# Optimization experiments

Measured on AMD Instinct MI355X. Metric: run time of the kernel, lower is better.

## Reference

```python
import jax, jax.numpy as jnp
import numpy as np

N_NODES = 100000
N_EDGES = 1600000
F_IN = 128
F_OUT = 64


def setup_inputs() -> dict:
    key = jax.random.key(0)
    kx, kw, kv, ks, kd = jax.random.split(key, 5)
    x = jax.random.normal(kx, (N_NODES, F_IN), dtype=jnp.float32)
    # xavier_uniform init for weight [in, out]
    limit = float(np.sqrt(6.0 / (F_IN + F_OUT)))
    weight = jax.random.uniform(kw, (F_IN, F_OUT), dtype=jnp.float32,
                                minval=-limit, maxval=limit)
    edge_val = jax.random.uniform(kv, (N_EDGES,), dtype=jnp.float32)
    edge_src = jax.random.randint(ks, (N_EDGES,), 0, N_NODES, dtype=jnp.int64)
    edge_dst = jax.random.randint(kd, (N_EDGES,), 0, N_NODES, dtype=jnp.int64)
    return {"x": x, "weight": weight, "edge_val": edge_val,
            "edge_src": edge_src, "edge_dst": edge_dst}


def reference(x, weight, edge_val, edge_src, edge_dst):
    # dropout p = 0.0 -> identity
    support = x @ weight                                  # [N, F_OUT] dense GEMM
    # spmm: out[dst] += val * support[src]  (adj row = dst, col = src)
    messages = support[edge_src] * edge_val[:, None]       # [E, F_OUT] gather
    out = jax.ops.segment_sum(messages, edge_dst,
                              num_segments=x.shape[0])     # [N, F_OUT] scatter-add
    return jax.nn.relu(out)
```

## Files before the change

### kernel.cpp

```cpp
#include <hip/hip_runtime.h>

#define F_IN 128
#define F_OUT 64
#define GROWS 128
#define XBSTRIDE 136

#define NPB 128
#define NPB_SHIFT 7
#define BCAP 800
#define ECAP 2240
#define TILE 8192
#define BSTH 1024
#define TMAX 256

__device__ inline unsigned f2bf(float f) {
    const unsigned u = __float_as_uint(f);
    return (u + 0x7FFFu + ((u >> 16) & 1u)) >> 16;
}
__device__ inline float bf_lo(unsigned u) { return __uint_as_float(u << 16); }
__device__ inline float bf_hi(unsigned u) { return __uint_as_float(u & 0xFFFF0000u); }

using bf16x8 = __attribute__((ext_vector_type(8))) short;
using f32x4  = __attribute__((ext_vector_type(4))) float;

struct GemmSh {
    unsigned short xt[GROWS * XBSTRIDE];
    unsigned short wth[F_OUT * XBSTRIDE];
    unsigned short wtl[F_OUT * XBSTRIDE];
};
struct ScatSh {
    int2 ebuf2[TILE];
    int  h[BCAP];
    int  lcur[BCAP];
    int  wsum[16];
    int  woff[16];
};
union FusedSh { GemmSh g; ScatSh s; };

__global__ __launch_bounds__(BSTH) void fused_kernel(const float* __restrict__ x,
                                                     const float* __restrict__ w,
                                                     unsigned short* __restrict__ support,
                                                     int n_nodes,
                                                     const float* __restrict__ edge_val,
                                                     const int* __restrict__ edge_src,
                                                     const int* __restrict__ edge_dst,
                                                     int* __restrict__ toff,
                                                     int2* __restrict__ sorted,
                                                     int n_edges, int nb, int T) {
    __shared__ FusedSh u;
    const int tid = threadIdx.x;

    if ((int)blockIdx.x >= T) {
        const int row0 = (blockIdx.x - T) * GROWS;

        {
            #pragma unroll
            for (int i = tid; i < F_OUT * (F_IN / 8); i += BSTH) {
                const int col = i & 63;
                const int kb  = (i >> 6) << 3;
                unsigned short sh[8], sl[8];
                #pragma unroll
                for (int j = 0; j < 8; ++j) {
                    const float f = w[(size_t)(kb + j) * F_OUT + col];
                    const unsigned h = f2bf(f);
                    sh[j] = (unsigned short)h;
                    sl[j] = (unsigned short)f2bf(f - __uint_as_float(h << 16));
                }
                uint4 oh, ol;
                oh.x = sh[0] | ((unsigned)sh[1] << 16); oh.y = sh[2] | ((unsigned)sh[3] << 16);
                oh.z = sh[4] | ((unsigned)sh[5] << 16); oh.w = sh[6] | ((unsigned)sh[7] << 16);
                ol.x = sl[0] | ((unsigned)sl[1] << 16); ol.y = sl[2] | ((unsigned)sl[3] << 16);
                ol.z = sl[4] | ((unsigned)sl[5] << 16); ol.w = sl[6] | ((unsigned)sl[7] << 16);
                *(uint4*)&u.g.wth[col * XBSTRIDE + kb] = oh;
                *(uint4*)&u.g.wtl[col * XBSTRIDE + kb] = ol;
            }
        }
        {
            const float4* x4 = (const float4*)x;
            #pragma unroll
            for (int i = tid; i < GROWS * (F_IN / 8); i += BSTH) {
                const int r  = i >> 4;
                const int k8 = i & 15;
                const int row = row0 + r;
                float4 a = make_float4(0.f, 0.f, 0.f, 0.f);
                float4 b = make_float4(0.f, 0.f, 0.f, 0.f);
                if (row < n_nodes) {
                    a = x4[(size_t)row * (F_IN / 4) + 2 * k8 + 0];
                    b = x4[(size_t)row * (F_IN / 4) + 2 * k8 + 1];
                }
                uint4 o;
                o.x = f2bf(a.x) | (f2bf(a.y) << 16);
                o.y = f2bf(a.z) | (f2bf(a.w) << 16);
                o.z = f2bf(b.x) | (f2bf(b.y) << 16);
                o.w = f2bf(b.z) | (f2bf(b.w) << 16);
                *(uint4*)&u.g.xt[r * XBSTRIDE + k8 * 8] = o;
            }
        }
        __syncthreads();

        const int ln = tid & 63;
        const int wv = tid >> 6;
        const int rt = wv >> 1;
        const int cp = (wv & 1) << 1;
        const int lr = ln >> 4;
        const int lc = ln & 15;

        const unsigned short* ar  = &u.g.xt [(rt * 16 + lc) * XBSTRIDE + lr * 8];
        const unsigned short* bh0 = &u.g.wth[(cp * 16 + lc) * XBSTRIDE + lr * 8];
        const unsigned short* bh1 = &u.g.wth[((cp + 1) * 16 + lc) * XBSTRIDE + lr * 8];
        const unsigned short* bl0 = &u.g.wtl[(cp * 16 + lc) * XBSTRIDE + lr * 8];
        const unsigned short* bl1 = &u.g.wtl[((cp + 1) * 16 + lc) * XBSTRIDE + lr * 8];

        f32x4 acc0 = {0.f, 0.f, 0.f, 0.f};
        f32x4 acc1 = {0.f, 0.f, 0.f, 0.f};
        #pragma unroll
        for (int kc = 0; kc < 4; ++kc) {
            const bf16x8 a  = *(const bf16x8*)(ar  + kc * 32);
            const bf16x8 h0 = *(const bf16x8*)(bh0 + kc * 32);
            const bf16x8 h1 = *(const bf16x8*)(bh1 + kc * 32);
            const bf16x8 l0 = *(const bf16x8*)(bl0 + kc * 32);
            const bf16x8 l1 = *(const bf16x8*)(bl1 + kc * 32);
            acc0 = __builtin_amdgcn_mfma_f32_16x16x32_bf16(a, h0, acc0, 0, 0, 0);
            acc1 = __builtin_amdgcn_mfma_f32_16x16x32_bf16(a, h1, acc1, 0, 0, 0);
            acc0 = __builtin_amdgcn_mfma_f32_16x16x32_bf16(a, l0, acc0, 0, 0, 0);
            acc1 = __builtin_amdgcn_mfma_f32_16x16x32_bf16(a, l1, acc1, 0, 0, 0);
        }

        #pragma unroll
        for (int i = 0; i < 4; ++i) {
            const int row = row0 + rt * 16 + lr * 4 + i;
            if (row < n_nodes) {
                unsigned short* sp = &support[(size_t)row * F_OUT + lc];
                sp[cp * 16]       = (unsigned short)f2bf(acc0[i]);
                sp[(cp + 1) * 16] = (unsigned short)f2bf(acc1[i]);
            }
        }
        return;
    }

    const int te  = blockIdx.x * TILE;
    const int cnt = min(TILE, n_edges - te);

    for (int i = tid; i < BCAP; i += BSTH) u.s.h[i] = 0;
    __syncthreads();

    const int cnt4 = cnt >> 2;
    const int4*   s4 = (const int4*)(edge_src + te);
    const int4*   d4 = (const int4*)(edge_dst + te);
    const float4* v4 = (const float4*)(edge_val + te);
    int4 rs[2], rd[2]; float4 rv[2];
    #pragma unroll
    for (int it = 0; it < 2; ++it) {
        const int t = tid + it * BSTH;
        if (t < cnt4) {
            rs[it] = s4[t]; rd[it] = d4[t]; rv[it] = v4[t];
            atomicAdd(&u.s.h[rd[it].x >> NPB_SHIFT], 1);
            atomicAdd(&u.s.h[rd[it].y >> NPB_SHIFT], 1);
            atomicAdd(&u.s.h[rd[it].z >> NPB_SHIFT], 1);
            atomicAdd(&u.s.h[rd[it].w >> NPB_SHIFT], 1);
        }
    }
    if (tid == 0) {
        for (int e = cnt4 << 2; e < cnt; ++e)
            atomicAdd(&u.s.h[edge_dst[te + e] >> NPB_SHIFT], 1);
    }
    __syncthreads();

    const int v = (tid < nb) ? u.s.h[tid] : 0;
    int s = v;
    #pragma unroll
    for (int off = 1; off < 64; off <<= 1) {
        const int t = __shfl_up(s, off, 64);
        if ((tid & 63) >= off) s += t;
    }
    const int wave = tid >> 6;
    if ((tid & 63) == 63) u.s.wsum[wave] = s;
    __syncthreads();
    if (tid < 16) {
        const int ws = u.s.wsum[tid];
        int sc = ws;
        #pragma unroll
        for (int off = 1; off < 16; off <<= 1) {
            const int t = __shfl_up(sc, off, 64);
            if (tid >= off) sc += t;
        }
        u.s.woff[tid] = sc - ws;
    }
    __syncthreads();

    {
        const int bid = blockIdx.x;
        if (tid < nb) {
            const int start = s + u.s.woff[wave] - v;
            u.s.lcur[tid] = start;
            toff[(size_t)tid * T + bid] = start;
        }
        if (tid == 0) toff[(size_t)nb * T + bid] = cnt;
    }
    __syncthreads();

    #pragma unroll
    for (int it = 0; it < 2; ++it) {
        const int t = tid + it * BSTH;
        if (t < cnt4) {
            int b, r;
            b = rd[it].x >> NPB_SHIFT; r = atomicAdd(&u.s.lcur[b], 1);
            u.s.ebuf2[r] = make_int2(rs[it].x | ((rd[it].x & (NPB - 1)) << 20), __float_as_int(rv[it].x));
            b = rd[it].y >> NPB_SHIFT; r = atomicAdd(&u.s.lcur[b], 1);
            u.s.ebuf2[r] = make_int2(rs[it].y | ((rd[it].y & (NPB - 1)) << 20), __float_as_int(rv[it].y));
            b = rd[it].z >> NPB_SHIFT; r = atomicAdd(&u.s.lcur[b], 1);
            u.s.ebuf2[r] = make_int2(rs[it].z | ((rd[it].z & (NPB - 1)) << 20), __float_as_int(rv[it].z));
            b = rd[it].w >> NPB_SHIFT; r = atomicAdd(&u.s.lcur[b], 1);
            u.s.ebuf2[r] = make_int2(rs[it].w | ((rd[it].w & (NPB - 1)) << 20), __float_as_int(rv[it].w));
        }
    }
    if (tid == 0) {
        for (int e = cnt4 << 2; e < cnt; ++e) {
            const int dd = edge_dst[te + e];
            const int b = dd >> NPB_SHIFT;
            const int r = atomicAdd(&u.s.lcur[b], 1);
            u.s.ebuf2[r] = make_int2(edge_src[te + e] | ((dd & (NPB - 1)) << 20),
                                     __float_as_int(edge_val[te + e]));
        }
    }
    __syncthreads();

    for (int k = tid; k < cnt; k += BSTH)
        sorted[(size_t)te + k] = u.s.ebuf2[k];
}

__global__ __launch_bounds__(512) void baccum_kernel(const unsigned short* __restrict__ support,
                                                     const int2* __restrict__ sorted,
                                                     const int* __restrict__ toff,
                                                     float* __restrict__ out,
                                                     int n_nodes, int T, int nb) {
    __shared__ int2 ebuf[ECAP];
    __shared__ int2 ebuf2[ECAP];
    __shared__ int tstart[TMAX];
    __shared__ int toffb[TMAX];
    __shared__ int tlen_s[TMAX];
    __shared__ int wsum3[4];
    __shared__ int total_s;
    __shared__ int hist[NPB];
    __shared__ int node_off[NPB + 1];
    __shared__ int cursor[NPB];
    __shared__ int wsum2[2];

    const int tid = threadIdx.x;
    const int b = blockIdx.x;

    int mycnt = 0, myoff = 0;
    if (tid < TMAX) {
        if (tid < T) {
            const int s0 = toff[(size_t)b * T + tid];
            const int e0 = toff[(size_t)(b + 1) * T + tid];
            toffb[tid] = s0;
            mycnt = e0 - s0;
            tlen_s[tid] = mycnt;
        }
        int s = mycnt;
        #pragma unroll
        for (int off = 1; off < 64; off <<= 1) {
            const int t = __shfl_up(s, off, 64);
            if ((tid & 63) >= off) s += t;
        }
        if ((tid & 63) == 63) wsum3[tid >> 6] = s;
        myoff = s - mycnt;
    }
    __syncthreads();
    if (tid < TMAX && tid < T) {
        int add = 0;
        const int wv = tid >> 6;
        for (int q2 = 0; q2 < wv; ++q2) add += wsum3[q2];
        tstart[tid] = myoff + add;
    }
    if (tid == 0) total_s = wsum3[0] + wsum3[1] + wsum3[2] + wsum3[3];
    __syncthreads();
    const int total = total_s;

    const int g8 = tid >> 3;
    const int q  = tid & 7;
    const uint4* sup = (const uint4*)support;

    float4 accA[2], accB[2];
    #pragma unroll
    for (int j = 0; j < 2; ++j) {
        accA[j] = make_float4(0.f, 0.f, 0.f, 0.f);
        accB[j] = make_float4(0.f, 0.f, 0.f, 0.f);
    }

    auto scan_bins = [&]() {
        int v = 0;
        if (tid < NPB) v = hist[tid];
        int s = v;
        if (tid < NPB) {
            #pragma unroll
            for (int off = 1; off < 64; off <<= 1) {
                const int t = __shfl_up(s, off, 64);
                if ((tid & 63) >= off) s += t;
            }
            if ((tid & 63) == 63) wsum2[tid >> 6] = s;
        }
        __syncthreads();
        if (tid < NPB) {
            const int incl = s + ((tid >= 64) ? wsum2[0] : 0);
            node_off[tid + 1] = incl;
            cursor[tid] = incl - v;
            if (tid == 0) node_off[0] = 0;
        }
    };
    auto gather = [&]() {
        #pragma unroll
        for (int j = 0; j < 2; ++j) {
            const int nl = g8 + 64 * j;
            int k = node_off[nl];
            const int ke = node_off[nl + 1];
            float4 aA = accA[j], aB = accB[j];
            while (k + 8 <= ke) {
                int2 e[8];
                uint4 s8[8];
                #pragma unroll
                for (int u2 = 0; u2 < 8; ++u2) e[u2] = ebuf2[k + u2];
                #pragma unroll
                for (int u2 = 0; u2 < 8; ++u2)
                    s8[u2] = sup[(size_t)(e[u2].x & 0xFFFFF) * 8 + q];
                #pragma unroll
                for (int u2 = 0; u2 < 8; ++u2) {
                    const float v = __int_as_float(e[u2].y);
                    aA.x += v * bf_lo(s8[u2].x); aA.y += v * bf_hi(s8[u2].x);
                    aA.z += v * bf_lo(s8[u2].y); aA.w += v * bf_hi(s8[u2].y);
                    aB.x += v * bf_lo(s8[u2].z); aB.y += v * bf_hi(s8[u2].z);
                    aB.z += v * bf_lo(s8[u2].w); aB.w += v * bf_hi(s8[u2].w);
                }
                k += 8;
            }
            for (; k < ke; ++k) {
                const int2 e0 = ebuf2[k];
                const uint4 s0 = sup[(size_t)(e0.x & 0xFFFFF) * 8 + q];
                const float v0 = __int_as_float(e0.y);
                aA.x += v0 * bf_lo(s0.x); aA.y += v0 * bf_hi(s0.x);
                aA.z += v0 * bf_lo(s0.y); aA.w += v0 * bf_hi(s0.y);
                aB.x += v0 * bf_lo(s0.z); aB.y += v0 * bf_hi(s0.z);
                aB.z += v0 * bf_lo(s0.w); aB.w += v0 * bf_hi(s0.w);
            }
            accA[j] = aA; accB[j] = aB;
        }
    };

    if (total <= ECAP) {
        if (tid < NPB) hist[tid] = 0;
        __syncthreads();

        const int wv = tid >> 6;
        const int ln = tid & 63;

        for (int t = wv; t < T; t += 8) {
            const int len = tlen_s[t];
            const size_t gbase = (size_t)t * TILE + toffb[t];
            for (int j = ln; j < len; j += 64) {
                const int2 ev = sorted[gbase + j];
                atomicAdd(&hist[((unsigned)ev.x) >> 20], 1);
            }
        }
        __syncthreads();

        scan_bins();
        __syncthreads();

        for (int t = wv; t < T; t += 8) {
            const int len = tlen_s[t];
            const size_t gbase = (size_t)t * TILE + toffb[t];
            for (int j = ln; j < len; j += 64) {
                const int2 ev = sorted[gbase + j];
                const int r = atomicAdd(&cursor[((unsigned)ev.x) >> 20], 1);
                ebuf2[r] = ev;
            }
        }
        __syncthreads();

        gather();
    } else {
        for (int cb = 0; cb < total; cb += ECAP) {
            const int cnt = min(ECAP, total - cb);

            __syncthreads();
            if (tid < NPB) hist[tid] = 0;
            __syncthreads();

            for (int i = tid; i < cnt; i += 512) {
                const int g = cb + i;
                int lo = 0, hi = T - 1;
                while (lo < hi) {
                    const int mid = (lo + hi + 1) >> 1;
                    if (tstart[mid] <= g) lo = mid; else hi = mid - 1;
                }
                const int2 ev = sorted[(size_t)lo * TILE + toffb[lo] + (g - tstart[lo])];
                ebuf[i] = ev;
                atomicAdd(&hist[((unsigned)ev.x) >> 20], 1);
            }
            __syncthreads();

            scan_bins();
            __syncthreads();

            for (int i = tid; i < cnt; i += 512) {
                const int2 ev = ebuf[i];
                const int r = atomicAdd(&cursor[((unsigned)ev.x) >> 20], 1);
                ebuf2[r] = ev;
            }
            __syncthreads();

            gather();
        }
    }

    const int base = b << NPB_SHIFT;
    #pragma unroll
    for (int j = 0; j < 2; ++j) {
        const int node = base + g8 + 64 * j;
        if (node < n_nodes) {
            float4 vA = accA[j], vB = accB[j];
            vA.x = fmaxf(vA.x, 0.f); vA.y = fmaxf(vA.y, 0.f);
            vA.z = fmaxf(vA.z, 0.f); vA.w = fmaxf(vA.w, 0.f);
            vB.x = fmaxf(vB.x, 0.f); vB.y = fmaxf(vB.y, 0.f);
            vB.z = fmaxf(vB.z, 0.f); vB.w = fmaxf(vB.w, 0.f);
            ((float4*)out)[(size_t)node * 16 + 2 * q + 0] = vA;
            ((float4*)out)[(size_t)node * 16 + 2 * q + 1] = vB;
        }
    }
}

__global__ __launch_bounds__(256) void scatter_kernel(const unsigned short* __restrict__ support,
                                                      const float* __restrict__ edge_val,
                                                      const int* __restrict__ edge_src,
                                                      const int* __restrict__ edge_dst,
                                                      float* __restrict__ out,
                                                      int n_edges) {
    const long gid = (long)blockIdx.x * blockDim.x + threadIdx.x;
    const int e = (int)(gid >> 4);
    if (e >= n_edges) return;
    const int q = (int)(gid & 15);
    const int src   = edge_src[e];
    const int dst   = edge_dst[e];
    const float val = edge_val[e];
    const uint2 s = ((const uint2*)support)[(size_t)src * 16 + q];
    float* o = &out[(size_t)dst * F_OUT + q * 4];
    atomicAdd(o + 0, val * bf_lo(s.x));
    atomicAdd(o + 1, val * bf_hi(s.x));
    atomicAdd(o + 2, val * bf_lo(s.y));
    atomicAdd(o + 3, val * bf_hi(s.y));
}

__global__ __launch_bounds__(256) void relu_kernel(float* __restrict__ out, int n4) {
    const int i = blockIdx.x * blockDim.x + threadIdx.x;
    if (i < n4) {
        float4 v = ((float4*)out)[i];
        v.x = fmaxf(v.x, 0.f); v.y = fmaxf(v.y, 0.f);
        v.z = fmaxf(v.z, 0.f); v.w = fmaxf(v.w, 0.f);
        ((float4*)out)[i] = v;
    }
}

extern "C" void kernel_launch(void* const* d_in, const int* in_sizes, int n_in,
                              void* d_out, int out_size, void* d_ws, size_t ws_size,
                              hipStream_t stream) {
    const float* x        = (const float*)d_in[0];
    const float* w        = (const float*)d_in[1];
    const float* edge_val = (const float*)d_in[2];
    const int*   edge_src = (const int*)d_in[3];
    const int*   edge_dst = (const int*)d_in[4];
    float* out = (float*)d_out;

    const int n_nodes = in_sizes[0] / F_IN;
    const int n_edges = in_sizes[2];
    const int nb = (n_nodes + NPB - 1) >> NPB_SHIFT;
    const int T  = (n_edges + TILE - 1) / TILE;
    const int G  = (n_nodes + GROWS - 1) / GROWS;

    char* p = (char*)d_ws;
    unsigned short* support = (unsigned short*)p;
    p += (size_t)n_nodes * F_OUT * sizeof(unsigned short);
    p = (char*)(((size_t)p + 15) & ~(size_t)15);
    int2* sorted = (int2*)p;  p += (size_t)T * TILE * sizeof(int2);
    int*  toff   = (int*)p;   p += (size_t)(nb + 1) * T * sizeof(int);
    const size_t ws_needed = (size_t)(p - (char*)d_ws);

    const bool ok = (ws_size >= ws_needed) && (nb <= BCAP) && (n_nodes < (1 << 20))
                    && (T <= TMAX);
    if (ok) {
        fused_kernel<<<T + G, BSTH, 0, stream>>>(x, w, support, n_nodes,
                                                 edge_val, edge_src, edge_dst,
                                                 toff, sorted, n_edges, nb, T);
        baccum_kernel<<<nb, 512, 0, stream>>>(support, sorted, toff, out,
                                              n_nodes, T, nb);
    } else {
        fused_kernel<<<G, BSTH, 0, stream>>>(x, w, support, n_nodes,
                                             edge_val, edge_src, edge_dst,
                                             nullptr, nullptr, n_edges, nb, 0);
        hipMemsetAsync(d_out, 0, (size_t)out_size * sizeof(float), stream);
        const long st = (long)n_edges * 16;
        scatter_kernel<<<(int)((st + 255) / 256), 256, 0, stream>>>(
            support, edge_val, edge_src, edge_dst, out, n_edges);
        const int n4o = out_size / 4;
        relu_kernel<<<(n4o + 255) / 256, 256, 0, stream>>>(out, n4o);
    }
}
```

Baseline: 176.9 us.

## Balance per-node gather with dynamic work queue and flat tile-map edge load

In the common fast path, each block now builds a byte map from edge position to source tile. This lets all threads load edges with a single flat, coalesced loop that reads global memory once into shared memory, instead of reading it twice with per-wave tile loops. The fixed assignment of two nodes per 8-thread group is replaced by an atomic counter, so groups pull nodes dynamically to even out imbalance caused by varying node degree. The tile map is filled serially per tile by one thread each, and the per-node atomic adds a little overhead.

```diff
diff --git a/kernel.cpp b/kernel.cpp
--- a/kernel.cpp
+++ b/kernel.cpp
@@ -236,6 +236,7 @@
                                                      int n_nodes, int T, int nb) {
     __shared__ int2 ebuf[ECAP];
     __shared__ int2 ebuf2[ECAP];
+    __shared__ unsigned char tileof[ECAP];
     __shared__ int tstart[TMAX];
     __shared__ int toffb[TMAX];
     __shared__ int tlen_s[TMAX];
@@ -245,6 +246,7 @@
     __shared__ int node_off[NPB + 1];
     __shared__ int cursor[NPB];
     __shared__ int wsum2[2];
+    __shared__ int next_node;
 
     const int tid = threadIdx.x;
     const int b = blockIdx.x;
@@ -274,20 +276,14 @@
         for (int q2 = 0; q2 < wv; ++q2) add += wsum3[q2];
         tstart[tid] = myoff + add;
     }
-    if (tid == 0) total_s = wsum3[0] + wsum3[1] + wsum3[2] + wsum3[3];
+    if (tid == 0) { total_s = wsum3[0] + wsum3[1] + wsum3[2] + wsum3[3]; next_node = 0; }
     __syncthreads();
     const int total = total_s;
 
     const int g8 = tid >> 3;
     const int q  = tid & 7;
+    const int ln = tid & 63;
     const uint4* sup = (const uint4*)support;
-
-    float4 accA[2], accB[2];
-    #pragma unroll
-    for (int j = 0; j < 2; ++j) {
-        accA[j] = make_float4(0.f, 0.f, 0.f, 0.f);
-        accB[j] = make_float4(0.f, 0.f, 0.f, 0.f);
-    }
 
     auto scan_bins = [&]() {
         int v = 0;
@@ -309,7 +305,122 @@
             if (tid == 0) node_off[0] = 0;
         }
     };
-    auto gather = [&]() {
+
+    if (total <= ECAP) {
+        if (tid < NPB) hist[tid] = 0;
+        for (int t = tid; t < T; t += 512) {
+            const int s0 = tstart[t];
+            const int len = tlen_s[t];
+            for (int j2 = 0; j2 < len; ++j2) tileof[s0 + j2] = (unsigned char)t;
+        }
+        __syncthreads();
+
+        for (int i = tid; i < total; i += 512) {
+            const int t = (int)tileof[i];
+            const int2 ev = sorted[(size_t)t * TILE + toffb[t] + (i - tstart[t])];
+            ebuf[i] = ev;
+            atomicAdd(&hist[((unsigned)ev.x) >> 20], 1);
+        }
+        __syncthreads();
+
+        scan_bins();
+        __syncthreads();
+
+        for (int i = tid; i < total; i += 512) {
+            const int2 ev = ebuf[i];
+            const int r = atomicAdd(&cursor[((unsigned)ev.x) >> 20], 1);
+            ebuf2[r] = ev;
+        }
+        __syncthreads();
+
+        while (true) {
+            int n = 0;
+            if (q == 0) n = atomicAdd(&next_node, 1);
+            n = __shfl(n, ln & ~7, 64);
+            if (n >= NPB) break;
+
+            int k = node_off[n];
+            const int ke = node_off[n + 1];
+            float4 aA = make_float4(0.f, 0.f, 0.f, 0.f);
+            float4 aB = make_float4(0.f, 0.f, 0.f, 0.f);
+            while (k + 8 <= ke) {
+                int2 e[8];
+                uint4 s8[8];
+                #pragma unroll
+                for (int u2 = 0; u2 < 8; ++u2) e[u2] = ebuf2[k + u2];
+                #pragma unroll
+                for (int u2 = 0; u2 < 8; ++u2)
+                    s8[u2] = sup[(size_t)(e[u2].x & 0xFFFFF) * 8 + q];
+                #pragma unroll
+                for (int u2 = 0; u2 < 8; ++u2) {
+                    const float v = __int_as_float(e[u2].y);
+                    aA.x += v * bf_lo(s8[u2].x); aA.y += v * bf_hi(s8[u2].x);
+                    aA.z += v * bf_lo(s8[u2].y); aA.w += v * bf_hi(s8[u2].y);
+                    aB.x += v * bf_lo(s8[u2].z); aB.y += v * bf_hi(s8[u2].z);
+                    aB.z += v * bf_lo(s8[u2].w); aB.w += v * bf_hi(s8[u2].w);
+                }
+                k += 8;
+            }
+            for (; k < ke; ++k) {
+                const int2 e0 = ebuf2[k];
+                const uint4 s0 = sup[(size_t)(e0.x & 0xFFFFF) * 8 + q];
+                const float v0 = __int_as_float(e0.y);
+                aA.x += v0 * bf_lo(s0.x); aA.y += v0 * bf_hi(s0.x);
+                aA.z += v0 * bf_lo(s0.y); aA.w += v0 * bf_hi(s0.y);
+                aB.x += v0 * bf_lo(s0.z); aB.y += v0 * bf_hi(s0.z);
+                aB.z += v0 * bf_lo(s0.w); aB.w += v0 * bf_hi(s0.w);
+            }
+
+            const int node = (b << NPB_SHIFT) + n;
+            if (node < n_nodes) {
+                aA.x = fmaxf(aA.x, 0.f); aA.y = fmaxf(aA.y, 0.f);
+                aA.z = fmaxf(aA.z, 0.f); aA.w = fmaxf(aA.w, 0.f);
+                aB.x = fmaxf(aB.x, 0.f); aB.y = fmaxf(aB.y, 0.f);
+                aB.z = fmaxf(aB.z, 0.f); aB.w = fmaxf(aB.w, 0.f);
+                ((float4*)out)[(size_t)node * 16 + 2 * q + 0] = aA;
+                ((float4*)out)[(size_t)node * 16 + 2 * q + 1] = aB;
+            }
+        }
+        return;
+    }
+
+    float4 accA[2], accB[2];
+    #pragma unroll
+    for (int j = 0; j < 2; ++j) {
+        accA[j] = make_float4(0.f, 0.f, 0.f, 0.f);
+        accB[j] = make_float4(0.f, 0.f, 0.f, 0.f);
+    }
+
+    for (int cb = 0; cb < total; cb += ECAP) {
+        const int cnt = min(ECAP, total - cb);
+
+        __syncthreads();
+        if (tid < NPB) hist[tid] = 0;
+        __syncthreads();
+
+        for (int i = tid; i < cnt; i += 512) {
+            const int g = cb + i;
+            int lo = 0, hi = T - 1;
+            while (lo < hi) {
+                const int mid = (lo + hi + 1) >> 1;
+                if (tstart[mid] <= g) lo = mid; else hi = mid - 1;
+            }
+            const int2 ev = sorted[(size_t)lo * TILE + toffb[lo] + (g - tstart[lo])];
+            ebuf[i] = ev;
+            atomicAdd(&hist[((unsigned)ev.x) >> 20], 1);
+        }
+        __syncthreads();
+
+        scan_bins();
+        __syncthreads();
+
+        for (int i = tid; i < cnt; i += 512) {
+            const int2 ev = ebuf[i];
+            const int r = atomicAdd(&cursor[((unsigned)ev.x) >> 20], 1);
+            ebuf2[r] = ev;
+        }
+        __syncthreads();
+
         #pragma unroll
         for (int j = 0; j < 2; ++j) {
             const int nl = g8 + 64 * j;
@@ -344,73 +455,6 @@
                 aB.z += v0 * bf_lo(s0.w); aB.w += v0 * bf_hi(s0.w);
             }
             accA[j] = aA; accB[j] = aB;
-        }
-    };
-
-    if (total <= ECAP) {
-        if (tid < NPB) hist[tid] = 0;
-        __syncthreads();
-
-        const int wv = tid >> 6;
-        const int ln = tid & 63;
-
-        for (int t = wv; t < T; t += 8) {
-            const int len = tlen_s[t];
-            const size_t gbase = (size_t)t * TILE + toffb[t];
-            for (int j = ln; j < len; j += 64) {
-                const int2 ev = sorted[gbase + j];
-                atomicAdd(&hist[((unsigned)ev.x) >> 20], 1);
-            }
-        }
-        __syncthreads();
-
-        scan_bins();
-        __syncthreads();
-
-        for (int t = wv; t < T; t += 8) {
-            const int len = tlen_s[t];
-            const size_t gbase = (size_t)t * TILE + toffb[t];
-            for (int j = ln; j < len; j += 64) {
-                const int2 ev = sorted[gbase + j];
-                const int r = atomicAdd(&cursor[((unsigned)ev.x) >> 20], 1);
-                ebuf2[r] = ev;
-            }
-        }
-        __syncthreads();
-
-        gather();
-    } else {
-        for (int cb = 0; cb < total; cb += ECAP) {
-            const int cnt = min(ECAP, total - cb);
-
-            __syncthreads();
-            if (tid < NPB) hist[tid] = 0;
-            __syncthreads();
-
-            for (int i = tid; i < cnt; i += 512) {
-                const int g = cb + i;
-                int lo = 0, hi = T - 1;
-                while (lo < hi) {
-                    const int mid = (lo + hi + 1) >> 1;
-                    if (tstart[mid] <= g) lo = mid; else hi = mid - 1;
-                }
-                const int2 ev = sorted[(size_t)lo * TILE + toffb[lo] + (g - tstart[lo])];
-                ebuf[i] = ev;
-                atomicAdd(&hist[((unsigned)ev.x) >> 20], 1);
-            }
-            __syncthreads();
-
-            scan_bins();
-            __syncthreads();
-
-            for (int i = tid; i < cnt; i += 512) {
-                const int2 ev = ebuf[i];
-                const int r = atomicAdd(&cursor[((unsigned)ev.x) >> 20], 1);
-                ebuf2[r] = ev;
-            }
-            __syncthreads();
-
-            gather();
         }
     }
 
```

Result: faster. 153.3 us (median of 2 runs) (-13.3%).
